# Optimization experiments

Hardware: AMD Instinct MI355X
Metric: run time of the kernel (lower is better)

The kernel has to match this reference:

```python
import jax, jax.numpy as jnp
import numpy as np

NUM_TOKENS = 32000
EMB_DIM = 1024
HID_DIM = 1024
NUM_LAYERS = 2
SEQ_LEN = 128
BATCH = 32


def setup_inputs() -> dict:
    key = jax.random.key(0)
    ks = jax.random.split(key, 8)
    initrange = 0.1
    stdv = 1.0 / np.sqrt(HID_DIM)  # torch nn.RNN default init: U(-1/sqrt(H), 1/sqrt(H))
    input_x = jax.random.randint(ks[0], (SEQ_LEN, BATCH), 0, NUM_TOKENS, dtype=jnp.int32)
    hidden = jnp.zeros((NUM_LAYERS, BATCH, HID_DIM), dtype=jnp.float32)
    emb = jax.random.uniform(ks[1], (NUM_TOKENS, EMB_DIM), jnp.float32, -initrange, initrange)
    # layer 0 input dim == EMB_DIM == HID_DIM, so stack per-layer weights
    W_ih = jax.random.uniform(ks[2], (NUM_LAYERS, HID_DIM, HID_DIM), jnp.float32, -stdv, stdv)
    W_hh = jax.random.uniform(ks[3], (NUM_LAYERS, HID_DIM, HID_DIM), jnp.float32, -stdv, stdv)
    b_ih = jax.random.uniform(ks[4], (NUM_LAYERS, HID_DIM), jnp.float32, -stdv, stdv)
    b_hh = jax.random.uniform(ks[5], (NUM_LAYERS, HID_DIM), jnp.float32, -stdv, stdv)
    W_out = jax.random.uniform(ks[6], (NUM_TOKENS, HID_DIM), jnp.float32, -initrange, initrange)
    b_out = jnp.zeros((NUM_TOKENS,), dtype=jnp.float32)
    return {"input_x": input_x, "hidden": hidden, "emb": emb, "W_ih": W_ih,
            "W_hh": W_hh, "b_ih": b_ih, "b_hh": b_hh, "W_out": W_out, "b_out": b_out}


def _run_layer(x_seq, h0, Wi, Wh, bi, bh):
    # x_seq: [T, B, E]; h0: [B, H]; tanh RNN recurrence
    xW = jnp.einsum('tbe,he->tbh', x_seq, Wi) + bi  # precompute input projection

    def step(h, x_t):
        h = jnp.tanh(x_t + h @ Wh.T + bh)
        return h, h

    hT, ys = jax.lax.scan(step, h0, xW)
    return ys, hT


def reference(input_x, hidden, emb, W_ih, W_hh, b_ih, b_hh, W_out, b_out):
    x = emb[input_x]  # [T, B, E]
    h_finals = []
    for l in range(NUM_LAYERS):
        x, hT = _run_layer(x, hidden[l], W_ih[l], W_hh[l], b_ih[l], b_hh[l])
        h_finals.append(hT)
    new_hidden = jnp.stack(h_finals, axis=0)  # [L, B, H]
    logits = jnp.einsum('tbh,vh->tbv', x, W_out) + b_out  # [T, B, V]
    logits = logits.reshape(-1, NUM_TOKENS)
    out = jax.nn.log_softmax(logits, axis=1)
    return out, new_hidden
```

## Files before the change

### kernel.cpp

```cpp
#include <hip/hip_runtime.h>
#include <cstdint>
#include <cstddef>

#define GLOBAL_AS __attribute__((address_space(1)))
#define LDS_AS    __attribute__((address_space(3)))

typedef _Float16 half4v __attribute__((ext_vector_type(4)));
typedef _Float16 half8v __attribute__((ext_vector_type(8)));
typedef float    f32x4  __attribute__((ext_vector_type(4)));

#define T_SEQ 128
#define NBATCH 32
#define HID   1024
#define VOCAB 32000
#define MROWS (T_SEQ * NBATCH)
#define RNN_WGS 16


__device__ __forceinline__ void load16_to_lds(const _Float16* gp, _Float16* lp) {
    __builtin_amdgcn_global_load_lds((const GLOBAL_AS uint32_t*)gp,
                                     (LDS_AS uint32_t*)lp, 16, 0, 0);
}

__device__ __forceinline__ float fast_tanh(float x) {
    float cx = fminf(fmaxf(x, -9.0f), 9.0f);
    float e2 = __expf(2.0f * cx);
    return (e2 - 1.0f) * __builtin_amdgcn_rcpf(e2 + 1.0f);
}


__global__ __launch_bounds__(256) void cvt_f32_f16(const float4* __restrict__ src,
                                                   half4v* __restrict__ dst, int n4) {
    int i = blockIdx.x * 256 + threadIdx.x;
    int stride = gridDim.x * 256;
    for (; i < n4; i += stride) {
        float4 v = src[i];
        half4v h = {(_Float16)v.x, (_Float16)v.y, (_Float16)v.z, (_Float16)v.w};
        dst[i] = h;
    }
}

__global__ __launch_bounds__(256) void gather_x(const int* __restrict__ ix,
                                                const float4* __restrict__ emb4,
                                                half4v* __restrict__ x4) {
    int r = blockIdx.x;
    int t = threadIdx.x;
    int tok = ix[r];
    float4 v = emb4[(size_t)tok * 256 + t];
    half4v h = {(_Float16)v.x, (_Float16)v.y, (_Float16)v.z, (_Float16)v.w};
    x4[(size_t)r * 256 + t] = h;
}

__global__ __launch_bounds__(256) void hf_init(const float* __restrict__ hidden,
                                               half8v* __restrict__ hf_l0,
                                               half8v* __restrict__ hf_l1,
                                               int* __restrict__ flags) {
    int idx = blockIdx.x * 256 + threadIdx.x;
    int l   = idx >> 12;
    int r   = idx & 4095;
    int kt   = r >> 7;
    int mt   = (r >> 6) & 1;
    int lane = r & 63;
    int b  = mt * 16 + (lane & 15);
    int k0 = kt * 32 + (lane >> 4) * 8;
    const float* s = hidden + ((size_t)l << 15) + ((size_t)b << 10) + k0;
    half8v h;
#pragma unroll
    for (int e = 0; e < 8; ++e) h[e] = (_Float16)s[e];
    (l ? hf_l1 : hf_l0)[r] = h;
    if (idx < 2 * T_SEQ) flags[idx] = 0;
}

__global__ __launch_bounds__(256) void gemm_f16_bt(const _Float16* __restrict__ A,
                                                   const _Float16* __restrict__ B,
                                                   const float* __restrict__ bias,
                                                   float* __restrict__ C,
                                                   int M, int N, int K) {
    __shared__ __align__(16) _Float16 As[128 * 32];
    __shared__ __align__(16) _Float16 Bs[128 * 32];
    const int t    = threadIdx.x;
    const int lane = t & 63;
    const int wave = t >> 6;
    const int wm   = (wave >> 1) << 6;
    const int wn   = (wave & 1) << 6;
    const int lr   = lane & 15;
    const int quad = lane >> 4;
    const long mBase = (long)blockIdx.y << 7;
    const long nBase = (long)blockIdx.x << 7;

    const int srow = t >> 2;
    const int scol = (t & 3) << 3;
    const _Float16* gA0 = A + (mBase + srow) * (long)K + scol;
    const _Float16* gA1 = A + (mBase + srow + 64) * (long)K + scol;
    const _Float16* gB0 = B + (nBase + srow) * (long)K + scol;
    const _Float16* gB1 = B + (nBase + srow + 64) * (long)K + scol;
    _Float16* lA0 = As + t * 8;
    _Float16* lA1 = As + (t + 256) * 8;
    _Float16* lB0 = Bs + t * 8;
    _Float16* lB1 = Bs + (t + 256) * 8;

    f32x4 acc[4][4] = {};

    for (int k0 = 0; k0 < K; k0 += 32) {
        load16_to_lds(gA0 + k0, lA0);
        load16_to_lds(gA1 + k0, lA1);
        load16_to_lds(gB0 + k0, lB0);
        load16_to_lds(gB1 + k0, lB1);
        __syncthreads();

        half8v aF[4], bF[4];
#pragma unroll
        for (int i = 0; i < 4; ++i) {
            aF[i] = *(const half8v*)&As[(wm + i * 16 + lr) * 32 + quad * 8];
            bF[i] = *(const half8v*)&Bs[(wn + i * 16 + lr) * 32 + quad * 8];
        }
#pragma unroll
        for (int mi = 0; mi < 4; ++mi)
#pragma unroll
            for (int ni = 0; ni < 4; ++ni)
                acc[mi][ni] = __builtin_amdgcn_mfma_f32_16x16x32_f16(
                    aF[mi], bF[ni], acc[mi][ni], 0, 0, 0);
        __syncthreads();
    }

#pragma unroll
    for (int ni = 0; ni < 4; ++ni) {
        long col = nBase + wn + ni * 16 + lr;
        float bv = bias ? bias[col] : 0.0f;
#pragma unroll
        for (int mi = 0; mi < 4; ++mi) {
            long row0 = mBase + wm + mi * 16 + quad * 4;
#pragma unroll
            for (int r = 0; r < 4; ++r)
                C[(row0 + r) * (long)N + col] = acc[mi][ni][r] + bv;
        }
    }
}

__global__ __launch_bounds__(256, 1) void rnn_layer_mfma(
    const float* __restrict__ xw,
    const _Float16* __restrict__ wh,
    const float* __restrict__ bh,
    const half8v* __restrict__ hf0,
    half8v* __restrict__ hf1,
    _Float16* __restrict__ y,
    float* __restrict__ hT,
    int* __restrict__ flags)
{
    const int g    = blockIdx.x;
    const int tid  = threadIdx.x;
    const int w    = tid >> 6;
    const int lane = tid & 63;
    const int lr   = lane & 15;
    const int quad = lane >> 4;
    const int jbase = g << 6;

    __shared__ float red[4][32][68];

    half8v bF[4][8];
#pragma unroll
    for (int nt = 0; nt < 4; ++nt)
#pragma unroll
        for (int kk = 0; kk < 8; ++kk)
            bF[nt][kk] = *(const half8v*)&wh[(size_t)(jbase + nt * 16 + lr) * HID
                                             + ((8 * w + kk) * 32 + quad * 8)];

    const int rm = tid >> 3;
    const int rn = (tid & 7) << 3;
    float bhv[8];
#pragma unroll
    for (int e = 0; e < 8; ++e) bhv[e] = bh[jbase + rn + e];
    const int houtIdx = ((2 * g + (rn >> 5)) * 2 + (rm >> 4)) * 64
                        + ((rn >> 3) & 3) * 16 + (rm & 15);

    const half8v* hbuf[2] = {hf0, (const half8v*)hf1};
    half8v* hbufw[2] = {(half8v*)hf0, hf1};

    for (int t = 0; t < T_SEQ; ++t) {
        const half8v* __restrict__ hin = hbuf[t & 1];
        half8v* __restrict__ hout      = hbufw[(t + 1) & 1];

        const float* xr = xw + ((size_t)(t * NBATCH + rm) << 10) + jbase + rn;
        float xv[8];
#pragma unroll
        for (int e = 0; e < 8; ++e) xv[e] = xr[e];

        half8v aF[2][8];
#pragma unroll
        for (int mt = 0; mt < 2; ++mt)
#pragma unroll
            for (int kk = 0; kk < 8; ++kk)
                aF[mt][kk] = hin[((8 * w + kk) * 2 + mt) * 64 + lane];

        f32x4 acc[2][4] = {};
#pragma unroll
        for (int kk = 0; kk < 8; ++kk)
#pragma unroll
            for (int mt = 0; mt < 2; ++mt)
#pragma unroll
                for (int nt = 0; nt < 4; ++nt)
                    acc[mt][nt] = __builtin_amdgcn_mfma_f32_16x16x32_f16(
                        aF[mt][kk], bF[nt][kk], acc[mt][nt], 0, 0, 0);

#pragma unroll
        for (int mt = 0; mt < 2; ++mt)
#pragma unroll
            for (int nt = 0; nt < 4; ++nt)
#pragma unroll
                for (int r = 0; r < 4; ++r)
                    red[w][mt * 16 + quad * 4 + r][nt * 16 + lr] = acc[mt][nt][r];
        __syncthreads();

        float v[8];
#pragma unroll
        for (int e = 0; e < 8; ++e) {
            float s = red[0][rm][rn + e] + red[1][rm][rn + e]
                    + red[2][rm][rn + e] + red[3][rm][rn + e];
            v[e] = fast_tanh(s + xv[e] + bhv[e]);
        }
        half8v hv;
#pragma unroll
        for (int e = 0; e < 8; ++e) hv[e] = (_Float16)v[e];
        *(half8v*)&y[((size_t)(t * NBATCH + rm) << 10) + jbase + rn] = hv;
        hout[houtIdx] = hv;
        if (t == T_SEQ - 1) {
#pragma unroll
            for (int e = 0; e < 8; ++e)
                hT[((size_t)rm << 10) + jbase + rn + e] = v[e];
        }

        __threadfence();
        if (tid == 0) {
            __hip_atomic_fetch_add(&flags[t], 1, __ATOMIC_RELEASE,
                                   __HIP_MEMORY_SCOPE_AGENT);
            while (__hip_atomic_load(&flags[t], __ATOMIC_RELAXED,
                                     __HIP_MEMORY_SCOPE_AGENT) < RNN_WGS)
                __builtin_amdgcn_s_sleep(1);
        }
        __syncthreads();
        __threadfence();
    }
}

__global__ __launch_bounds__(256) void logsoftmax_rows(float* __restrict__ logits) {
    const long r = blockIdx.x;
    float4* row = (float4*)(logits + r * (long)VOCAB);
    __shared__ float red[256];
    const int t = threadIdx.x;

    float m = -3.4e38f;
    for (int i = t; i < 8000; i += 256) {
        float4 v = row[i];
        m = fmaxf(m, fmaxf(fmaxf(v.x, v.y), fmaxf(v.z, v.w)));
    }
    red[t] = m; __syncthreads();
    for (int o = 128; o > 0; o >>= 1) {
        if (t < o) red[t] = fmaxf(red[t], red[t + o]);
        __syncthreads();
    }
    m = red[0]; __syncthreads();

    float s = 0.0f;
    for (int i = t; i < 8000; i += 256) {
        float4 v = row[i];
        s += __expf(v.x - m) + __expf(v.y - m) + __expf(v.z - m) + __expf(v.w - m);
    }
    red[t] = s; __syncthreads();
    for (int o = 128; o > 0; o >>= 1) {
        if (t < o) red[t] += red[t + o];
        __syncthreads();
    }
    const float lse = m + __logf(red[0]);

    for (int i = t; i < 8000; i += 256) {
        float4 v = row[i];
        v.x -= lse; v.y -= lse; v.z -= lse; v.w -= lse;
        row[i] = v;
    }
}


extern "C" void kernel_launch(void* const* d_in, const int* in_sizes, int n_in,
                              void* d_out, int out_size, void* d_ws, size_t ws_size,
                              hipStream_t stream) {
    const int*   ix    = (const int*)  d_in[0];
    const float* hid0  = (const float*)d_in[1];
    const float* emb   = (const float*)d_in[2];
    const float* W_ih  = (const float*)d_in[3];
    const float* W_hh  = (const float*)d_in[4];
    const float* b_ih  = (const float*)d_in[5];
    const float* b_hh  = (const float*)d_in[6];
    const float* W_out = (const float*)d_in[7];
    const float* b_out = (const float*)d_in[8];

    float* logits = (float*)d_out;
    float* hidT   = logits + (size_t)MROWS * VOCAB;

    char* ws = (char*)d_ws;
    _Float16* Wi_h   = (_Float16*)ws;  ws += (size_t)2 * 1024 * 1024 * sizeof(_Float16);
    _Float16* Wout_h = (_Float16*)ws;  ws += (size_t)VOCAB * 1024 * sizeof(_Float16);
    _Float16* Wh_h   = (_Float16*)ws;  ws += (size_t)2 * 1024 * 1024 * sizeof(_Float16);
    _Float16* x_h    = (_Float16*)ws;  ws += (size_t)MROWS * 1024 * sizeof(_Float16);
    _Float16* y_h    = (_Float16*)ws;  ws += (size_t)MROWS * 1024 * sizeof(_Float16);
    float*    xw     = (float*)ws;     ws += (size_t)MROWS * 1024 * sizeof(float);

    char* sc = (char*)d_out;
    half8v* hfA = (half8v*)sc;
    half8v* hfB = (half8v*)(sc + 65536);
    half8v* hfC = (half8v*)(sc + 131072);
    half8v* hfD = (half8v*)(sc + 196608);
    int*    flags = (int*)(sc + 262144);

    cvt_f32_f16<<<2048, 256, 0, stream>>>((const float4*)W_ih, (half4v*)Wi_h,
                                          2 * 1024 * 1024 / 4);
    cvt_f32_f16<<<8192, 256, 0, stream>>>((const float4*)W_out, (half4v*)Wout_h,
                                          VOCAB * 1024 / 4);
    cvt_f32_f16<<<2048, 256, 0, stream>>>((const float4*)W_hh, (half4v*)Wh_h,
                                          2 * 1024 * 1024 / 4);
    gather_x<<<MROWS, 256, 0, stream>>>(ix, (const float4*)emb, (half4v*)x_h);
    hf_init<<<32, 256, 0, stream>>>(hid0, hfA, hfC, flags);

    dim3 g1(HID / 128, MROWS / 128);
    gemm_f16_bt<<<g1, 256, 0, stream>>>(x_h, Wi_h, b_ih, xw, MROWS, HID, HID);
    rnn_layer_mfma<<<RNN_WGS, 256, 0, stream>>>(xw, Wh_h, b_hh, hfA, hfB,
                                                y_h, hidT, flags);
    gemm_f16_bt<<<g1, 256, 0, stream>>>(y_h, Wi_h + 1024 * 1024, b_ih + 1024, xw,
                                        MROWS, HID, HID);
    rnn_layer_mfma<<<RNN_WGS, 256, 0, stream>>>(xw, Wh_h + 1024 * 1024, b_hh + 1024,
                                                hfC, hfD, x_h, hidT + 32 * 1024,
                                                flags + T_SEQ);
    dim3 g3(VOCAB / 128, MROWS / 128);
    gemm_f16_bt<<<g3, 256, 0, stream>>>(x_h, Wout_h, b_out, logits, MROWS, VOCAB, HID);
    logsoftmax_rows<<<MROWS, 256, 0, stream>>>(logits);
}
```

Before: 3.260 ms.

## Replace atomic grid barrier with per-wave epoch flags in persistent RNN kernel

After: 2.922 ms. 1.12x faster.

```diff
diff --git a/kernel.cpp b/kernel.cpp
--- a/kernel.cpp
+++ b/kernel.cpp
@@ -8,6 +8,7 @@
 typedef _Float16 half4v __attribute__((ext_vector_type(4)));
 typedef _Float16 half8v __attribute__((ext_vector_type(8)));
 typedef float    f32x4  __attribute__((ext_vector_type(4)));
+typedef uint32_t u32x4  __attribute__((ext_vector_type(4)));
 
 #define T_SEQ 128
 #define NBATCH 32
@@ -68,7 +69,7 @@
 #pragma unroll
     for (int e = 0; e < 8; ++e) h[e] = (_Float16)s[e];
     (l ? hf_l1 : hf_l0)[r] = h;
-    if (idx < 2 * T_SEQ) flags[idx] = 0;
+    if (idx < 256) flags[idx] = 0;
 }
 
 __global__ __launch_bounds__(256) void gemm_f16_bt(const _Float16* __restrict__ A,
@@ -141,7 +142,7 @@
     const float* __restrict__ xw,
     const _Float16* __restrict__ wh,
     const float* __restrict__ bh,
-    const half8v* __restrict__ hf0,
+    half8v* __restrict__ hf0,
     half8v* __restrict__ hf1,
     _Float16* __restrict__ y,
     float* __restrict__ hT,
@@ -155,15 +156,20 @@
     const int quad = lane >> 4;
     const int jbase = g << 6;
 
-    __shared__ float red[4][32][68];
-
-    half8v bF[4][8];
+    __shared__ float red[4][32][72];
+
+    u32x4 bF[4][8];
 #pragma unroll
     for (int nt = 0; nt < 4; ++nt)
 #pragma unroll
-        for (int kk = 0; kk < 8; ++kk)
-            bF[nt][kk] = *(const half8v*)&wh[(size_t)(jbase + nt * 16 + lr) * HID
-                                             + ((8 * w + kk) * 32 + quad * 8)];
+        for (int kk = 0; kk < 8; ++kk) {
+            const void* p = &wh[(size_t)(jbase + nt * 16 + lr) * HID
+                                + ((8 * w + kk) * 32 + quad * 8)];
+            asm volatile("global_load_dwordx4 %0, %1, off"
+                         : "=v"(bF[nt][kk]) : "v"(p));
+        }
+    asm volatile("s_waitcnt vmcnt(0)" ::: "memory");
+    __builtin_amdgcn_sched_barrier(0);
 
     const int rm = tid >> 3;
     const int rn = (tid & 7) << 3;
@@ -173,24 +179,28 @@
     const int houtIdx = ((2 * g + (rn >> 5)) * 2 + (rm >> 4)) * 64
                         + ((rn >> 3) & 3) * 16 + (rm & 15);
 
-    const half8v* hbuf[2] = {hf0, (const half8v*)hf1};
-    half8v* hbufw[2] = {(half8v*)hf0, hf1};
+    float xv[8];
+    {
+        const float* xr = xw + ((size_t)rm << 10) + jbase + rn;
+#pragma unroll
+        for (int e = 0; e < 8; ++e) xv[e] = xr[e];
+    }
+
+    const u32x4* hin = (const u32x4*)hf0;
+    u32x4*       hout = (u32x4*)hf1;
 
     for (int t = 0; t < T_SEQ; ++t) {
-        const half8v* __restrict__ hin = hbuf[t & 1];
-        half8v* __restrict__ hout      = hbufw[(t + 1) & 1];
-
-        const float* xr = xw + ((size_t)(t * NBATCH + rm) << 10) + jbase + rn;
-        float xv[8];
-#pragma unroll
-        for (int e = 0; e < 8; ++e) xv[e] = xr[e];
-
-        half8v aF[2][8];
-#pragma unroll
-        for (int mt = 0; mt < 2; ++mt)
-#pragma unroll
-            for (int kk = 0; kk < 8; ++kk)
-                aF[mt][kk] = hin[((8 * w + kk) * 2 + mt) * 64 + lane];
+        u32x4 aF[2][8];
+#pragma unroll
+        for (int kk = 0; kk < 8; ++kk)
+#pragma unroll
+            for (int mt = 0; mt < 2; ++mt) {
+                const void* p = hin + ((8 * w + kk) * 2 + mt) * 64 + lane;
+                asm volatile("global_load_dwordx4 %0, %1, off sc0 sc1"
+                             : "=v"(aF[mt][kk]) : "v"(p));
+            }
+        asm volatile("s_waitcnt vmcnt(0)" ::: "memory");
+        __builtin_amdgcn_sched_barrier(0);
 
         f32x4 acc[2][4] = {};
 #pragma unroll
@@ -200,7 +210,9 @@
 #pragma unroll
                 for (int nt = 0; nt < 4; ++nt)
                     acc[mt][nt] = __builtin_amdgcn_mfma_f32_16x16x32_f16(
-                        aF[mt][kk], bF[nt][kk], acc[mt][nt], 0, 0, 0);
+                        __builtin_bit_cast(half8v, aF[mt][kk]),
+                        __builtin_bit_cast(half8v, bF[nt][kk]),
+                        acc[mt][nt], 0, 0, 0);
 
 #pragma unroll
         for (int mt = 0; mt < 2; ++mt)
@@ -211,34 +223,63 @@
                     red[w][mt * 16 + quad * 4 + r][nt * 16 + lr] = acc[mt][nt][r];
         __syncthreads();
 
-        float v[8];
-#pragma unroll
-        for (int e = 0; e < 8; ++e) {
-            float s = red[0][rm][rn + e] + red[1][rm][rn + e]
-                    + red[2][rm][rn + e] + red[3][rm][rn + e];
-            v[e] = fast_tanh(s + xv[e] + bhv[e]);
-        }
+        float4 lo = *(const float4*)&red[0][rm][rn];
+        float4 hi = *(const float4*)&red[0][rm][rn + 4];
+#pragma unroll
+        for (int ww = 1; ww < 4; ++ww) {
+            float4 a = *(const float4*)&red[ww][rm][rn];
+            float4 b = *(const float4*)&red[ww][rm][rn + 4];
+            lo.x += a.x; lo.y += a.y; lo.z += a.z; lo.w += a.w;
+            hi.x += b.x; hi.y += b.y; hi.z += b.z; hi.w += b.w;
+        }
+        float v[8] = {lo.x, lo.y, lo.z, lo.w, hi.x, hi.y, hi.z, hi.w};
+#pragma unroll
+        for (int e = 0; e < 8; ++e) v[e] = fast_tanh(v[e] + xv[e] + bhv[e]);
         half8v hv;
 #pragma unroll
         for (int e = 0; e < 8; ++e) hv[e] = (_Float16)v[e];
+
+        {
+            u32x4 hq = __builtin_bit_cast(u32x4, hv);
+            void* p = hout + houtIdx;
+            asm volatile("global_store_dwordx4 %0, %1, off sc0 sc1"
+                         :: "v"(p), "v"(hq) : "memory");
+        }
+        asm volatile("s_waitcnt vmcnt(0)" ::: "memory");
+
+        if (lane == 0) {
+            int ep = t + 1;
+            asm volatile("global_store_dword %0, %1, off sc0 sc1"
+                         :: "v"(&flags[g * 4 + w]), "v"(ep) : "memory");
+        }
+
         *(half8v*)&y[((size_t)(t * NBATCH + rm) << 10) + jbase + rn] = hv;
-        hout[houtIdx] = hv;
+
         if (t == T_SEQ - 1) {
 #pragma unroll
             for (int e = 0; e < 8; ++e)
                 hT[((size_t)rm << 10) + jbase + rn + e] = v[e];
-        }
-
-        __threadfence();
-        if (tid == 0) {
-            __hip_atomic_fetch_add(&flags[t], 1, __ATOMIC_RELEASE,
-                                   __HIP_MEMORY_SCOPE_AGENT);
-            while (__hip_atomic_load(&flags[t], __ATOMIC_RELAXED,
-                                     __HIP_MEMORY_SCOPE_AGENT) < RNN_WGS)
-                __builtin_amdgcn_s_sleep(1);
-        }
-        __syncthreads();
-        __threadfence();
+        } else {
+            const float* xr = xw + ((size_t)((t + 1) * NBATCH + rm) << 10) + jbase + rn;
+            float xn[8];
+#pragma unroll
+            for (int e = 0; e < 8; ++e) xn[e] = xr[e];
+
+            int fv;
+            const int* fp = flags + lane;
+            do {
+                asm volatile("global_load_dword %0, %1, off sc0 sc1\n\t"
+                             "s_waitcnt vmcnt(0)"
+                             : "=v"(fv) : "v"(fp) : "memory");
+            } while (!__all(fv >= t + 1));
+
+#pragma unroll
+            for (int e = 0; e < 8; ++e) xv[e] = xn[e];
+        }
+
+        u32x4* tmp = (u32x4*)hin;
+        hin  = (const u32x4*)hout;
+        hout = tmp;
     }
 }
 
@@ -328,7 +369,7 @@
                                         MROWS, HID, HID);
     rnn_layer_mfma<<<RNN_WGS, 256, 0, stream>>>(xw, Wh_h + 1024 * 1024, b_hh + 1024,
                                                 hfC, hfD, x_h, hidT + 32 * 1024,
-                                                flags + T_SEQ);
+                                                flags + 64);
     dim3 g3(VOCAB / 128, MROWS / 128);
     gemm_f16_bt<<<g3, 256, 0, stream>>>(x_h, Wout_h, b_out, logits, MROWS, VOCAB, HID);
     logsoftmax_rows<<<MROWS, 256, 0, stream>>>(logits);
```
